# Optimization experiments

Hardware: AMD Instinct MI355X
Metric: run time of the kernel (lower is better)

## Reference

```python
import jax, jax.numpy as jnp
import numpy as np

EPS = 1e-8
NUM_GCN_LAYERS = 2


def _cos(a, b):
    # cosine similarity along last axis, torch.nn.CosineSimilarity semantics
    num = jnp.sum(a * b, axis=-1)
    den = jnp.maximum(jnp.linalg.norm(a, axis=-1) * jnp.linalg.norm(b, axis=-1), EPS)
    return num / den


def _masked_mean(x, mask):
    # x: [..., L, D], mask: [..., L]
    s = jnp.sum(x * mask[..., None], axis=-2)
    d = jnp.maximum(jnp.sum(mask, axis=-1, keepdims=True), 1.0)
    return s / d


def setup_inputs() -> dict:
    key = jax.random.key(0)
    ks = jax.random.split(key, 12)
    B, C, L, D, P, OM, OE, R = 32, 16, 128, 768, 196, 10, 10, 36
    return {
        "mention_text_feature": jax.random.normal(ks[0], (B, L, D), jnp.float32),
        "mention_text_mask": jnp.ones((B, L), jnp.float32),
        "mention_start_pos": jax.random.randint(ks[1], (B,), 0, L),
        "mention_end_pos": jax.random.randint(ks[2], (B,), 0, L),
        "mention_image_feature": jax.random.normal(ks[3], (B, P, D), jnp.float32),
        "mention_object_feature": jax.random.normal(ks[4], (B, OM, R, D), jnp.float32),
        "mention_object_score": jax.random.uniform(ks[5], (B, OM), jnp.float32, 0.1, 1.0),
        "entity_text_feature": jax.random.normal(ks[6], (B, C, L, D), jnp.float32),
        "entity_text_mask": jnp.ones((B, C, L), jnp.float32),
        "entity_image_feature": jax.random.normal(ks[7], (B, C, P, D), jnp.float32),
        "entity_object_feature": jax.random.normal(ks[8], (B, C, OE, R, D), jnp.float32),
        "entity_object_score": jax.random.uniform(ks[9], (B, C, OE), jnp.float32, 0.1, 1.0),
        "miet_similarity": jax.random.normal(ks[10], (B, C), jnp.float32),
        "mtei_similarity": jax.random.normal(ks[11], (B, C), jnp.float32),
    }


def _forward(mtf, mtm, msp, mep, mif, mof, mos, etf, etm, eif, eof, eos, miet, mtei):
    B, L, D = mtf.shape
    C = etf.shape[1]

    # ---- VertexEncoder ----
    v_mt = _masked_mean(mtf, mtm)      # [B, D] mention text vertex
    v_mi = jnp.mean(mif, axis=-2)      # [B, D] mention image vertex
    v_et = _masked_mean(etf, etm)      # [B, C, D] entity text vertex
    v_ei = jnp.mean(eif, axis=-2)      # [B, C, D] entity image vertex

    # ---- EdgeEncoder ----
    # mention final repr: mean of start/end token features (span boundary repr)
    start = jnp.take_along_axis(mtf, msp[:, None, None], axis=1)[:, 0]  # [B, D]
    end = jnp.take_along_axis(mtf, mep[:, None, None], axis=1)[:, 0]    # [B, D]
    m_span = 0.5 * (start + end)
    mtet = _cos(m_span[:, None, :], etf[:, :, 0])  # [B, C] vs entity CLS token

    # miei: the original double python loop over (i, j) object pairs is a
    # weighted average of pairwise cosine sims -> one fused einsum pass.
    m = jnp.mean(mof, axis=-2)         # [B, OM, D]
    e = jnp.mean(eof, axis=-2)         # [B, C, OE, D]
    mn = m / jnp.maximum(jnp.linalg.norm(m, axis=-1, keepdims=True), EPS)
    en = e / jnp.maximum(jnp.linalg.norm(e, axis=-1, keepdims=True), EPS)
    cos_ij = jnp.einsum('bid,bcjd->bcij', mn, en)          # [B, C, OM, OE]
    w = mos[:, None, :, None] * eos[:, :, None, :]          # [B, C, OM, OE]
    miei = jnp.sum(cos_ij * w, axis=(2, 3)) / jnp.sum(w, axis=(2, 3))  # [B, C]

    # ---- GCN layers ----
    edges = [jnp.broadcast_to(x[:, :, None], (B, C, D)) for x in (mtet, mtei, miet, miei)]
    vertexes = [v_mt, v_mi, v_et, v_ei]
    vertex_graph = [[(0, 2), (1, 3)], [(2, 2), (3, 3)], [(0, 0), (2, 1)], [(1, 0), (3, 1)]]
    edge_graph = [(0, 2), (0, 3), (1, 2), (1, 3)]

    def conv_v(edge, v, mention_like):
        msg = edge * (v[:, None, :] if v.ndim == 2 else v)  # [B, C, D]
        return jnp.mean(msg, axis=1) if mention_like else msg

    def conv_e(u, v):
        u2 = u[:, None, :] if u.ndim == 2 else u
        v2 = v[:, None, :] if v.ndim == 2 else v
        return u2 * v2  # [B, C, D]

    for _ in range(NUM_GCN_LAYERS):
        new_v = []
        for k, nbrs in enumerate(vertex_graph):
            mention_like = k < 2  # vertexes 0,1 are [B,D]; 2,3 are [B,C,D]
            acc = conv_v(edges[nbrs[0][0]], vertexes[nbrs[0][1]], mention_like)
            acc = acc + conv_v(edges[nbrs[1][0]], vertexes[nbrs[1][1]], mention_like)
            new_v.append(acc)
        new_e = [conv_e(vertexes[ui], vertexes[vi]) for ui, vi in edge_graph]
        vertexes, edges = new_v, new_e

    mention, entity = vertexes[0], vertexes[2]
    return _cos(mention[:, None, :], entity)  # [B, C]


def reference(mention_text_feature, mention_text_mask, mention_start_pos, mention_end_pos, mention_image_feature, mention_object_feature, mention_object_score, entity_text_feature, entity_text_mask, entity_image_feature, entity_object_feature, entity_object_score, miet_similarity, mtei_similarity):
    return _forward(mention_text_feature, mention_text_mask, mention_start_pos, mention_end_pos, mention_image_feature, mention_object_feature, mention_object_score, entity_text_feature, entity_text_mask, entity_image_feature, entity_object_feature, entity_object_score, miet_similarity, mtei_similarity)
```

## Files before the change

### kernel.cpp

```cpp
#include <hip/hip_runtime.h>

#define EPSF 1e-8f

#define B_  32
#define C_  16
#define L_  128
#define D_  768
#define D4_ 192
#define P_  196
#define OM_ 10
#define OE_ 10
#define R_  36

__device__ __forceinline__ float4 f4add(float4 a, float4 b){
  return make_float4(a.x+b.x, a.y+b.y, a.z+b.z, a.w+b.w);
}
__device__ __forceinline__ float4 f4scale(float4 a, float s){
  return make_float4(a.x*s, a.y*s, a.z*s, a.w*s);
}
__device__ __forceinline__ float f4dot(float4 a, float4 b){
  return a.x*b.x + a.y*b.y + a.z*b.z + a.w*b.w;
}
__device__ __forceinline__ float wave_sum(float v){
  #pragma unroll
  for (int off = 32; off > 0; off >>= 1) v += __shfl_down(v, off);
  return v;
}

__global__ __launch_bounds__(192)
void mof_k(const float* __restrict__ mof, const float* __restrict__ mos,
           float* __restrict__ m_mean, float* __restrict__ q)
{
  int blk = blockIdx.x;
  int t = threadIdx.x, wv = t >> 6, lane = t & 63;
  const float4* inp = (const float4*)mof + (size_t)blk * R_ * D4_;
  float4 acc = make_float4(0.f, 0.f, 0.f, 0.f);
  #pragma unroll 6
  for (int r = 0; r < R_; ++r)
    acc = f4add(acc, inp[(size_t)r * D4_ + t]);
  acc = f4scale(acc, 1.f / 36.f);
  ((float4*)m_mean)[(size_t)blk * D4_ + t] = acc;
  __shared__ float sh[3];
  float n = wave_sum(f4dot(acc, acc));
  if (lane == 0) sh[wv] = n;
  __syncthreads();
  if (t == 0) q[blk] = mos[blk] / fmaxf(sqrtf(sh[0] + sh[1] + sh[2]), EPSF);
}

__global__ __launch_bounds__(192)
void mega2_k(const float* __restrict__ eofp, const float* __restrict__ eif,
             const float* __restrict__ etf, const float* __restrict__ mif,
             const float* __restrict__ mtf,
             const float* __restrict__ etm, const float* __restrict__ mtm,
             const float* __restrict__ m_mean, const float* __restrict__ q,
             const float* __restrict__ eos,
             float* __restrict__ part_eif, float* __restrict__ part_etf,
             float* __restrict__ part_mif, float* __restrict__ part_mtf,
             float* __restrict__ msum, float* __restrict__ p)
{
  int blk = blockIdx.x;
  int t = threadIdx.x;

  if (blk < 1707) {
    int wave = t >> 6, lane = t & 63;
    int g = blk * 3 + wave;
    if (g >= 5120) return;
    int b = g / (C_ * OE_);
    const float4* ep = (const float4*)eofp + (size_t)g * R_ * D4_;
    float4 a0 = make_float4(0,0,0,0), a1 = a0, a2 = a0;
    #pragma unroll 4
    for (int r = 0; r < R_; ++r) {
      const float4* row = ep + (size_t)r * D4_;
      a0 = f4add(a0, row[lane]);
      a1 = f4add(a1, row[lane + 64]);
      a2 = f4add(a2, row[lane + 128]);
    }
    const float inv36 = 1.f / 36.f;
    a0 = f4scale(a0, inv36); a1 = f4scale(a1, inv36); a2 = f4scale(a2, inv36);
    float nrm = f4dot(a0, a0) + f4dot(a1, a1) + f4dot(a2, a2);
    float s = 0.f;
    const float4* mp = (const float4*)m_mean + (size_t)b * OM_ * D4_;
    #pragma unroll
    for (int i = 0; i < OM_; ++i) {
      const float4* mr = mp + (size_t)i * D4_;
      float di = f4dot(a0, mr[lane]) + f4dot(a1, mr[lane + 64]) + f4dot(a2, mr[lane + 128]);
      s += q[b * OM_ + i] * di;
    }
    s = wave_sum(s); nrm = wave_sum(nrm);
    if (lane == 0) p[g] = eos[g] * s / fmaxf(sqrtf(nrm), EPSF);
    return;
  }

  blk -= 1707;
  const float* in; const float* mask = nullptr;
  float* part; float* ms = nullptr;
  int ROWS, CH, RPC;
  if (blk < 3584)      { in = eif; part = part_eif; ROWS = 196; CH = 7; RPC = 28; }
  else if (blk < 5632) { blk -= 3584; in = etf; mask = etm; ms = msum + 128;
                         part = part_etf; ROWS = 128; CH = 4; RPC = 32; }
  else if (blk < 5856) { blk -= 5632; in = mif; part = part_mif; ROWS = 196; CH = 7; RPC = 28; }
  else                 { blk -= 5856; in = mtf; mask = mtm; ms = msum;
                         part = part_mtf; ROWS = 128; CH = 4; RPC = 32; }

  int g = blk / CH, ch = blk - g * CH;
  int r0 = ch * RPC;
  int r1 = r0 + RPC; if (r1 > ROWS) r1 = ROWS;
  const float4* inp = (const float4*)in + (size_t)g * ROWS * D4_;
  float4 acc = make_float4(0.f, 0.f, 0.f, 0.f);
  if (mask) {
    const float* mrow = mask + (size_t)g * ROWS;
    float msacc = 0.f;
    #pragma unroll 4
    for (int r = r0; r < r1; ++r) {
      float w = mrow[r];
      float4 v = inp[(size_t)r * D4_ + t];
      acc.x += v.x * w; acc.y += v.y * w; acc.z += v.z * w; acc.w += v.w * w;
      msacc += w;
    }
    if (t == 0) ms[blk] = msacc;
  } else {
    #pragma unroll 4
    for (int r = r0; r < r1; ++r)
      acc = f4add(acc, inp[(size_t)r * D4_ + t]);
  }
  ((float4*)part)[(size_t)blk * D4_ + t] = acc;
}

__device__ __forceinline__ void combine_body(const float* __restrict__ part,
                                             const float* __restrict__ msum,
                                             float* __restrict__ out,
                                             int secblk, int CH, float invn)
{
  int idx = secblk * 256 + threadIdx.x;
  int g = idx / D4_, t = idx - g * D4_;
  const float4* pp = (const float4*)part + (size_t)(g * CH) * D4_ + t;
  float4 acc = make_float4(0.f, 0.f, 0.f, 0.f);
  for (int ch = 0; ch < CH; ++ch) acc = f4add(acc, pp[(size_t)ch * D4_]);
  float scale;
  if (msum) {
    float s = 0.f;
    for (int ch = 0; ch < CH; ++ch) s += msum[g * CH + ch];
    scale = 1.f / fmaxf(s, 1.f);
  } else scale = invn;
  ((float4*)out)[idx] = f4scale(acc, scale);
}

__global__ __launch_bounds__(256)
void comb2_k(const float* __restrict__ part_eif, const float* __restrict__ part_etf,
             const float* __restrict__ part_mif, const float* __restrict__ part_mtf,
             const float* __restrict__ msum,
             const float* __restrict__ etf, const float* __restrict__ mtf,
             const int* __restrict__ msp, const int* __restrict__ mep,
             float* __restrict__ v_ei, float* __restrict__ v_et,
             float* __restrict__ v_mi, float* __restrict__ v_mt,
             float* __restrict__ mtet)
{
  int blk = blockIdx.x;
  if (blk < 384)       { combine_body(part_eif, nullptr, v_ei, blk, 7, 1.f/196.f); return; }
  else if (blk < 768)  { combine_body(part_etf, msum + 128, v_et, blk - 384, 4, 0.f); return; }
  else if (blk < 792)  { combine_body(part_mif, nullptr, v_mi, blk - 768, 7, 1.f/196.f); return; }
  else if (blk < 816)  { combine_body(part_mtf, msum, v_mt, blk - 792, 4, 0.f); return; }
  else {
    int w = (blk - 816) * 4 + (threadIdx.x >> 6);
    int lane = threadIdx.x & 63;
    int b = w >> 4;
    const float4* ecls = (const float4*)etf + (size_t)w * L_ * D4_;
    const float4* mb   = (const float4*)mtf + (size_t)b * L_ * D4_;
    int sp = msp[b], ep = mep[b];
    float dt = 0.f, na = 0.f, nb = 0.f;
    #pragma unroll
    for (int k = 0; k < 3; ++k) {
      float4 a = f4scale(f4add(mb[(size_t)sp * D4_ + lane + 64*k],
                               mb[(size_t)ep * D4_ + lane + 64*k]), 0.5f);
      float4 e = ecls[lane + 64*k];
      dt += f4dot(a, e); na += f4dot(a, a); nb += f4dot(e, e);
    }
    dt = wave_sum(dt); na = wave_sum(na); nb = wave_sum(nb);
    if (lane == 0) mtet[w] = dt / fmaxf(sqrtf(na) * sqrtf(nb), EPSF);
  }
}

__global__ __launch_bounds__(256)
void tail_k(const float* __restrict__ p, const float* __restrict__ mos,
            const float* __restrict__ eos,
            const float* __restrict__ v_mt, const float* __restrict__ v_mi,
            const float* __restrict__ v_et, const float* __restrict__ v_ei,
            const float* __restrict__ mtet, const float* __restrict__ mtei,
            const float* __restrict__ miet,
            float* __restrict__ out)
{
  __shared__ float sh_e0[C_], sh_e1[C_], sh_e2[C_], sh_e3[C_];
  __shared__ float4 sh_m4[D4_], sh_s4[D4_];
  int b = blockIdx.x, tid = threadIdx.x;

  if (tid < C_) {
    int bc = b * C_ + tid;
    float num = 0.f, se = 0.f, sm = 0.f;
    #pragma unroll
    for (int j = 0; j < OE_; ++j) { num += p[bc * OE_ + j]; se += eos[bc * OE_ + j]; }
    #pragma unroll
    for (int i = 0; i < OM_; ++i) sm += mos[b * OM_ + i];
    sh_e3[tid] = num / (sm * se);
    sh_e0[tid] = mtet[bc];
    sh_e1[tid] = mtei[bc];
    sh_e2[tid] = miet[bc];
  }
  __syncthreads();

  const float invC = 1.f / (float)C_;
  for (int d = tid; d < D_; d += 256) {
    float vmt = v_mt[b * D_ + d], vmi = v_mi[b * D_ + d];
    float nv0 = 0.f, nv1 = 0.f, macc = 0.f;
    #pragma unroll
    for (int c = 0; c < C_; ++c) {
      int bc = b * C_ + c;
      float et = v_et[(size_t)bc * D_ + d];
      float ei = v_ei[(size_t)bc * D_ + d];
      float e0 = sh_e0[c], e1 = sh_e1[c], e2 = sh_e2[c], e3 = sh_e3[c];
      nv0 += e0 * et + e1 * ei;
      nv1 += e2 * et + e3 * ei;
      macc += (vmt * et) * (e0 * vmt + e2 * vmi)
            + (vmt * ei) * (e1 * vmt + e3 * vmi);
    }
    ((float*)sh_m4)[d] = macc * invC;
    ((float*)sh_s4)[d] = vmt * (nv0 * invC) + vmi * (nv1 * invC);
  }
  __syncthreads();

  int wv = tid >> 6, lane = tid & 63;
  for (int c = wv; c < C_; c += 4) {
    const float4* ep = (const float4*)v_et + (size_t)(b * C_ + c) * D4_;
    float dt = 0.f, nm = 0.f, ne = 0.f;
    #pragma unroll
    for (int k = 0; k < 3; ++k) {
      float4 m = sh_m4[lane + 64*k];
      float4 sv = sh_s4[lane + 64*k];
      float4 e = ep[lane + 64*k];
      float4 ent = make_float4(e.x * sv.x, e.y * sv.y, e.z * sv.z, e.w * sv.w);
      dt += f4dot(m, ent); nm += f4dot(m, m); ne += f4dot(ent, ent);
    }
    dt = wave_sum(dt); nm = wave_sum(nm); ne = wave_sum(ne);
    if (lane == 0) out[b * C_ + c] = dt / fmaxf(sqrtf(nm) * sqrtf(ne), EPSF);
  }
}

extern "C" void kernel_launch(void* const* d_in, const int* in_sizes, int n_in,
                              void* d_out, int out_size, void* d_ws, size_t ws_size,
                              hipStream_t stream)
{
  const float* mtf  = (const float*)d_in[0];
  const float* mtm  = (const float*)d_in[1];
  const int*   msp  = (const int*)  d_in[2];
  const int*   mep  = (const int*)  d_in[3];
  const float* mif  = (const float*)d_in[4];
  const float* mof  = (const float*)d_in[5];
  const float* mos  = (const float*)d_in[6];
  const float* etf  = (const float*)d_in[7];
  const float* etm  = (const float*)d_in[8];
  const float* eif  = (const float*)d_in[9];
  const float* eofp = (const float*)d_in[10];
  const float* eos  = (const float*)d_in[11];
  const float* miet = (const float*)d_in[12];
  const float* mtei = (const float*)d_in[13];
  float* out = (float*)d_out;
  float* ws = (float*)d_ws;

  float* PART_EIF = ws;
  float* PART_ETF = PART_EIF + 2752512;
  float* PART_MIF = PART_ETF + 1572864;
  float* PART_MTF = PART_MIF + 172032;
  float* MSUM     = PART_MTF + 98304;
  float* M_MEAN   = MSUM     + 2176;
  float* Q        = M_MEAN   + 245760;
  float* V_MT     = Q        + 512;
  float* V_MI     = V_MT     + 24576;
  float* V_ET     = V_MI     + 24576;
  float* V_EI     = V_ET     + 393216;
  float* MTET     = V_EI     + 393216;
  float* P_BUF    = MTET     + 512;

  mof_k<<<320, 192, 0, stream>>>(mof, mos, M_MEAN, Q);

  mega2_k<<<7691, 192, 0, stream>>>(eofp, eif, etf, mif, mtf, etm, mtm,
                                    M_MEAN, Q, eos,
                                    PART_EIF, PART_ETF, PART_MIF, PART_MTF,
                                    MSUM, P_BUF);

  comb2_k<<<944, 256, 0, stream>>>(PART_EIF, PART_ETF, PART_MIF, PART_MTF,
                                   MSUM, etf, mtf, msp, mep,
                                   V_EI, V_ET, V_MI, V_MT, MTET);

  tail_k<<<B_, 256, 0, stream>>>(P_BUF, mos, eos, V_MT, V_MI, V_ET, V_EI,
                                 MTET, mtei, miet, out);
}
```

Measured before the change: 226.0 us.

## Restructure into three kernels with two-chunk partials and fused final combine

Moves the mention image/text means and the CLS cosine into the first kernel alongside the object means. The entity image and text reductions now use two chunks per group instead of 7 and 4. The separate combine kernel is removed: the last kernel sums the two partials directly, keeping entity text vertices in shared memory. All streaming reads use nontemporal loads. The aim is fewer launches and less partial-buffer traffic, at the cost of fewer blocks for the large reductions and a heavier final kernel running only 32 blocks.

```diff
diff --git a/kernel.cpp b/kernel.cpp
--- a/kernel.cpp
+++ b/kernel.cpp
@@ -12,77 +12,139 @@
 #define OE_ 10
 #define R_  36
 
-__device__ __forceinline__ float4 f4add(float4 a, float4 b){
-  return make_float4(a.x+b.x, a.y+b.y, a.z+b.z, a.w+b.w);
-}
-__device__ __forceinline__ float4 f4scale(float4 a, float s){
-  return make_float4(a.x*s, a.y*s, a.z*s, a.w*s);
-}
-__device__ __forceinline__ float f4dot(float4 a, float4 b){
-  return a.x*b.x + a.y*b.y + a.z*b.z + a.w*b.w;
-}
+typedef float f4 __attribute__((ext_vector_type(4)));
+
+__device__ __forceinline__ float f4dot(f4 a, f4 b){ return a.x*b.x + a.y*b.y + a.z*b.z + a.w*b.w; }
+__device__ __forceinline__ f4 ldnt(const f4* p){ return __builtin_nontemporal_load(p); }
 __device__ __forceinline__ float wave_sum(float v){
   #pragma unroll
   for (int off = 32; off > 0; off >>= 1) v += __shfl_down(v, off);
   return v;
 }
 
+__global__ __launch_bounds__(384)
+void d1_k(const float* __restrict__ mof, const float* __restrict__ mos,
+          const float* __restrict__ mif, const float* __restrict__ mtf,
+          const float* __restrict__ mtm, const float* __restrict__ etf,
+          const int* __restrict__ msp, const int* __restrict__ mep,
+          float* __restrict__ m_mean, float* __restrict__ q,
+          float* __restrict__ v_mi, float* __restrict__ v_mt,
+          float* __restrict__ mtet)
+{
+  __shared__ f4 shv[2][D4_];
+  __shared__ float shs[4];
+  int blk = blockIdx.x, t = threadIdx.x;
+
+  if (blk < 320) {
+    int g = blk;
+    int half = t / D4_, col = t - half * D4_;
+    const f4* base = (const f4*)mof + (size_t)g * R_ * D4_;
+    f4 acc = {0.f, 0.f, 0.f, 0.f};
+    int r0 = half * 18;
+    #pragma unroll 6
+    for (int r = r0; r < r0 + 18; ++r) acc += ldnt(base + (size_t)r * D4_ + col);
+    shv[half][col] = acc;
+    __syncthreads();
+    if (t < D4_) {
+      f4 mean = (shv[0][col] + shv[1][col]) * (1.f / 36.f);
+      ((f4*)m_mean)[(size_t)g * D4_ + col] = mean;
+      float n = wave_sum(f4dot(mean, mean));
+      if ((t & 63) == 0) shs[t >> 6] = n;
+    }
+    __syncthreads();
+    if (t == 0) q[g] = mos[g] / fmaxf(sqrtf(shs[0] + shs[1] + shs[2]), EPSF);
+    return;
+  }
+  if (blk < 352) {
+    int b = blk - 320;
+    int half = t / D4_, col = t - half * D4_;
+    const f4* base = (const f4*)mif + (size_t)b * P_ * D4_;
+    f4 acc = {0.f, 0.f, 0.f, 0.f};
+    int r0 = half * 98;
+    #pragma unroll 4
+    for (int r = r0; r < r0 + 98; ++r) acc += ldnt(base + (size_t)r * D4_ + col);
+    shv[half][col] = acc;
+    __syncthreads();
+    if (t < D4_)
+      ((f4*)v_mi)[(size_t)b * D4_ + col] = (shv[0][col] + shv[1][col]) * (1.f / 196.f);
+    return;
+  }
+  if (blk < 384) {
+    int b = blk - 352;
+    int half = t / D4_, col = t - half * D4_;
+    const f4* base = (const f4*)mtf + (size_t)b * L_ * D4_;
+    const float* mrow = mtm + (size_t)b * L_;
+    f4 acc = {0.f, 0.f, 0.f, 0.f};
+    float ms = 0.f;
+    int r0 = half * 64;
+    #pragma unroll 4
+    for (int r = r0; r < r0 + 64; ++r) {
+      float w = mrow[r];
+      acc += ldnt(base + (size_t)r * D4_ + col) * w;
+      ms += w;
+    }
+    shv[half][col] = acc;
+    if (t == 0)    shs[0] = ms;
+    if (t == D4_)  shs[1] = ms;
+    __syncthreads();
+    if (t < D4_) {
+      float scale = 1.f / fmaxf(shs[0] + shs[1], 1.f);
+      ((f4*)v_mt)[(size_t)b * D4_ + col] = (shv[0][col] + shv[1][col]) * scale;
+    }
+    return;
+  }
+  {
+    int w = (blk - 384) * 6 + (t >> 6);
+    if (w >= B_ * C_) return;
+    int lane = t & 63;
+    int b = w >> 4;
+    const f4* ecls = (const f4*)etf + (size_t)w * L_ * D4_;
+    const f4* mb   = (const f4*)mtf + (size_t)b * L_ * D4_;
+    int sp = msp[b], ep = mep[b];
+    float dt = 0.f, na = 0.f, nb = 0.f;
+    #pragma unroll
+    for (int k = 0; k < 3; ++k) {
+      f4 a = (mb[(size_t)sp * D4_ + lane + 64*k] + mb[(size_t)ep * D4_ + lane + 64*k]) * 0.5f;
+      f4 e = ecls[lane + 64*k];
+      dt += f4dot(a, e); na += f4dot(a, a); nb += f4dot(e, e);
+    }
+    dt = wave_sum(dt); na = wave_sum(na); nb = wave_sum(nb);
+    if (lane == 0) mtet[w] = dt / fmaxf(sqrtf(na) * sqrtf(nb), EPSF);
+  }
+}
+
 __global__ __launch_bounds__(192)
-void mof_k(const float* __restrict__ mof, const float* __restrict__ mos,
-           float* __restrict__ m_mean, float* __restrict__ q)
-{
-  int blk = blockIdx.x;
-  int t = threadIdx.x, wv = t >> 6, lane = t & 63;
-  const float4* inp = (const float4*)mof + (size_t)blk * R_ * D4_;
-  float4 acc = make_float4(0.f, 0.f, 0.f, 0.f);
-  #pragma unroll 6
-  for (int r = 0; r < R_; ++r)
-    acc = f4add(acc, inp[(size_t)r * D4_ + t]);
-  acc = f4scale(acc, 1.f / 36.f);
-  ((float4*)m_mean)[(size_t)blk * D4_ + t] = acc;
-  __shared__ float sh[3];
-  float n = wave_sum(f4dot(acc, acc));
-  if (lane == 0) sh[wv] = n;
-  __syncthreads();
-  if (t == 0) q[blk] = mos[blk] / fmaxf(sqrtf(sh[0] + sh[1] + sh[2]), EPSF);
-}
-
-__global__ __launch_bounds__(192)
-void mega2_k(const float* __restrict__ eofp, const float* __restrict__ eif,
-             const float* __restrict__ etf, const float* __restrict__ mif,
-             const float* __restrict__ mtf,
-             const float* __restrict__ etm, const float* __restrict__ mtm,
-             const float* __restrict__ m_mean, const float* __restrict__ q,
-             const float* __restrict__ eos,
-             float* __restrict__ part_eif, float* __restrict__ part_etf,
-             float* __restrict__ part_mif, float* __restrict__ part_mtf,
-             float* __restrict__ msum, float* __restrict__ p)
-{
-  int blk = blockIdx.x;
-  int t = threadIdx.x;
+void d2_k(const float* __restrict__ eofp, const float* __restrict__ eif,
+          const float* __restrict__ etf, const float* __restrict__ etm,
+          const float* __restrict__ m_mean, const float* __restrict__ q,
+          const float* __restrict__ eos,
+          float* __restrict__ part_eif, float* __restrict__ part_etf,
+          float* __restrict__ msum_etf, float* __restrict__ p)
+{
+  int blk = blockIdx.x, t = threadIdx.x;
 
   if (blk < 1707) {
     int wave = t >> 6, lane = t & 63;
     int g = blk * 3 + wave;
-    if (g >= 5120) return;
+    if (g >= B_ * C_ * OE_) return;
     int b = g / (C_ * OE_);
-    const float4* ep = (const float4*)eofp + (size_t)g * R_ * D4_;
-    float4 a0 = make_float4(0,0,0,0), a1 = a0, a2 = a0;
+    const f4* ep = (const f4*)eofp + (size_t)g * R_ * D4_;
+    f4 a0 = {0.f,0.f,0.f,0.f}, a1 = a0, a2 = a0;
     #pragma unroll 4
     for (int r = 0; r < R_; ++r) {
-      const float4* row = ep + (size_t)r * D4_;
-      a0 = f4add(a0, row[lane]);
-      a1 = f4add(a1, row[lane + 64]);
-      a2 = f4add(a2, row[lane + 128]);
+      const f4* row = ep + (size_t)r * D4_;
+      a0 += ldnt(row + lane);
+      a1 += ldnt(row + lane + 64);
+      a2 += ldnt(row + lane + 128);
     }
     const float inv36 = 1.f / 36.f;
-    a0 = f4scale(a0, inv36); a1 = f4scale(a1, inv36); a2 = f4scale(a2, inv36);
+    a0 *= inv36; a1 *= inv36; a2 *= inv36;
     float nrm = f4dot(a0, a0) + f4dot(a1, a1) + f4dot(a2, a2);
     float s = 0.f;
-    const float4* mp = (const float4*)m_mean + (size_t)b * OM_ * D4_;
+    const f4* mp = (const f4*)m_mean + (size_t)b * OM_ * D4_;
     #pragma unroll
     for (int i = 0; i < OM_; ++i) {
-      const float4* mr = mp + (size_t)i * D4_;
+      const f4* mr = mp + (size_t)i * D4_;
       float di = f4dot(a0, mr[lane]) + f4dot(a1, mr[lane + 64]) + f4dot(a2, mr[lane + 128]);
       s += q[b * OM_ + i] * di;
     }
@@ -90,153 +152,103 @@
     if (lane == 0) p[g] = eos[g] * s / fmaxf(sqrtf(nrm), EPSF);
     return;
   }
-
   blk -= 1707;
-  const float* in; const float* mask = nullptr;
-  float* part; float* ms = nullptr;
-  int ROWS, CH, RPC;
-  if (blk < 3584)      { in = eif; part = part_eif; ROWS = 196; CH = 7; RPC = 28; }
-  else if (blk < 5632) { blk -= 3584; in = etf; mask = etm; ms = msum + 128;
-                         part = part_etf; ROWS = 128; CH = 4; RPC = 32; }
-  else if (blk < 5856) { blk -= 5632; in = mif; part = part_mif; ROWS = 196; CH = 7; RPC = 28; }
-  else                 { blk -= 5856; in = mtf; mask = mtm; ms = msum;
-                         part = part_mtf; ROWS = 128; CH = 4; RPC = 32; }
-
-  int g = blk / CH, ch = blk - g * CH;
-  int r0 = ch * RPC;
-  int r1 = r0 + RPC; if (r1 > ROWS) r1 = ROWS;
-  const float4* inp = (const float4*)in + (size_t)g * ROWS * D4_;
-  float4 acc = make_float4(0.f, 0.f, 0.f, 0.f);
-  if (mask) {
-    const float* mrow = mask + (size_t)g * ROWS;
-    float msacc = 0.f;
-    #pragma unroll 4
-    for (int r = r0; r < r1; ++r) {
+  if (blk < 1024) {
+    int g = blk >> 1, ch = blk & 1;
+    const f4* inp = (const f4*)eif + ((size_t)g * P_ + ch * 98) * D4_;
+    f4 acc = {0.f,0.f,0.f,0.f};
+    #pragma unroll 4
+    for (int r = 0; r < 98; ++r) acc += ldnt(inp + (size_t)r * D4_ + t);
+    ((f4*)part_eif)[(size_t)blk * D4_ + t] = acc;
+    return;
+  }
+  blk -= 1024;
+  {
+    int g = blk >> 1, ch = blk & 1;
+    const f4* inp = (const f4*)etf + ((size_t)g * L_ + ch * 64) * D4_;
+    const float* mrow = etm + (size_t)g * L_ + ch * 64;
+    f4 acc = {0.f,0.f,0.f,0.f};
+    float ms = 0.f;
+    #pragma unroll 4
+    for (int r = 0; r < 64; ++r) {
       float w = mrow[r];
-      float4 v = inp[(size_t)r * D4_ + t];
-      acc.x += v.x * w; acc.y += v.y * w; acc.z += v.z * w; acc.w += v.w * w;
-      msacc += w;
-    }
-    if (t == 0) ms[blk] = msacc;
-  } else {
-    #pragma unroll 4
-    for (int r = r0; r < r1; ++r)
-      acc = f4add(acc, inp[(size_t)r * D4_ + t]);
-  }
-  ((float4*)part)[(size_t)blk * D4_ + t] = acc;
-}
-
-__device__ __forceinline__ void combine_body(const float* __restrict__ part,
-                                             const float* __restrict__ msum,
-                                             float* __restrict__ out,
-                                             int secblk, int CH, float invn)
-{
-  int idx = secblk * 256 + threadIdx.x;
-  int g = idx / D4_, t = idx - g * D4_;
-  const float4* pp = (const float4*)part + (size_t)(g * CH) * D4_ + t;
-  float4 acc = make_float4(0.f, 0.f, 0.f, 0.f);
-  for (int ch = 0; ch < CH; ++ch) acc = f4add(acc, pp[(size_t)ch * D4_]);
-  float scale;
-  if (msum) {
-    float s = 0.f;
-    for (int ch = 0; ch < CH; ++ch) s += msum[g * CH + ch];
-    scale = 1.f / fmaxf(s, 1.f);
-  } else scale = invn;
-  ((float4*)out)[idx] = f4scale(acc, scale);
-}
-
-__global__ __launch_bounds__(256)
-void comb2_k(const float* __restrict__ part_eif, const float* __restrict__ part_etf,
-             const float* __restrict__ part_mif, const float* __restrict__ part_mtf,
-             const float* __restrict__ msum,
-             const float* __restrict__ etf, const float* __restrict__ mtf,
-             const int* __restrict__ msp, const int* __restrict__ mep,
-             float* __restrict__ v_ei, float* __restrict__ v_et,
-             float* __restrict__ v_mi, float* __restrict__ v_mt,
-             float* __restrict__ mtet)
-{
-  int blk = blockIdx.x;
-  if (blk < 384)       { combine_body(part_eif, nullptr, v_ei, blk, 7, 1.f/196.f); return; }
-  else if (blk < 768)  { combine_body(part_etf, msum + 128, v_et, blk - 384, 4, 0.f); return; }
-  else if (blk < 792)  { combine_body(part_mif, nullptr, v_mi, blk - 768, 7, 1.f/196.f); return; }
-  else if (blk < 816)  { combine_body(part_mtf, msum, v_mt, blk - 792, 4, 0.f); return; }
-  else {
-    int w = (blk - 816) * 4 + (threadIdx.x >> 6);
-    int lane = threadIdx.x & 63;
-    int b = w >> 4;
-    const float4* ecls = (const float4*)etf + (size_t)w * L_ * D4_;
-    const float4* mb   = (const float4*)mtf + (size_t)b * L_ * D4_;
-    int sp = msp[b], ep = mep[b];
-    float dt = 0.f, na = 0.f, nb = 0.f;
-    #pragma unroll
-    for (int k = 0; k < 3; ++k) {
-      float4 a = f4scale(f4add(mb[(size_t)sp * D4_ + lane + 64*k],
-                               mb[(size_t)ep * D4_ + lane + 64*k]), 0.5f);
-      float4 e = ecls[lane + 64*k];
-      dt += f4dot(a, e); na += f4dot(a, a); nb += f4dot(e, e);
-    }
-    dt = wave_sum(dt); na = wave_sum(na); nb = wave_sum(nb);
-    if (lane == 0) mtet[w] = dt / fmaxf(sqrtf(na) * sqrtf(nb), EPSF);
-  }
-}
-
-__global__ __launch_bounds__(256)
-void tail_k(const float* __restrict__ p, const float* __restrict__ mos,
-            const float* __restrict__ eos,
-            const float* __restrict__ v_mt, const float* __restrict__ v_mi,
-            const float* __restrict__ v_et, const float* __restrict__ v_ei,
-            const float* __restrict__ mtet, const float* __restrict__ mtei,
-            const float* __restrict__ miet,
-            float* __restrict__ out)
-{
+      acc += ldnt(inp + (size_t)r * D4_ + t) * w;
+      ms += w;
+    }
+    ((f4*)part_etf)[(size_t)blk * D4_ + t] = acc;
+    if (t == 0) msum_etf[blk] = ms;
+  }
+}
+
+__global__ __launch_bounds__(384)
+void d3_k(const float* __restrict__ part_eif, const float* __restrict__ part_etf,
+          const float* __restrict__ msum_etf,
+          const float* __restrict__ p, const float* __restrict__ mos,
+          const float* __restrict__ eos,
+          const float* __restrict__ v_mt, const float* __restrict__ v_mi,
+          const float* __restrict__ mtet, const float* __restrict__ mtei,
+          const float* __restrict__ miet,
+          float* __restrict__ out)
+{
+  __shared__ float s_vet[C_][D_];
   __shared__ float sh_e0[C_], sh_e1[C_], sh_e2[C_], sh_e3[C_];
-  __shared__ float4 sh_m4[D4_], sh_s4[D4_];
-  int b = blockIdx.x, tid = threadIdx.x;
-
-  if (tid < C_) {
-    int bc = b * C_ + tid;
+  __shared__ float sh_m[D_], sh_s[D_];
+  int b = blockIdx.x, t = threadIdx.x;
+
+  for (int it = t; it < C_ * D4_; it += 384) {
+    int c = it / D4_, col = it - c * D4_;
+    int i2 = (b * C_ + c) * 2;
+    f4 a = ((const f4*)part_etf)[(size_t)i2 * D4_ + col]
+         + ((const f4*)part_etf)[(size_t)(i2 + 1) * D4_ + col];
+    float scale = 1.f / fmaxf(msum_etf[i2] + msum_etf[i2 + 1], 1.f);
+    ((f4*)&s_vet[c][0])[col] = a * scale;
+  }
+  if (t < C_) {
+    int bc = b * C_ + t;
     float num = 0.f, se = 0.f, sm = 0.f;
     #pragma unroll
     for (int j = 0; j < OE_; ++j) { num += p[bc * OE_ + j]; se += eos[bc * OE_ + j]; }
     #pragma unroll
     for (int i = 0; i < OM_; ++i) sm += mos[b * OM_ + i];
-    sh_e3[tid] = num / (sm * se);
-    sh_e0[tid] = mtet[bc];
-    sh_e1[tid] = mtei[bc];
-    sh_e2[tid] = miet[bc];
+    sh_e3[t] = num / (sm * se);
+    sh_e0[t] = mtet[bc];
+    sh_e1[t] = mtei[bc];
+    sh_e2[t] = miet[bc];
   }
   __syncthreads();
 
-  const float invC = 1.f / (float)C_;
-  for (int d = tid; d < D_; d += 256) {
+  const float invC = 1.f / (float)C_, inv196 = 1.f / 196.f;
+  for (int d = t; d < D_; d += 384) {
     float vmt = v_mt[b * D_ + d], vmi = v_mi[b * D_ + d];
     float nv0 = 0.f, nv1 = 0.f, macc = 0.f;
     #pragma unroll
     for (int c = 0; c < C_; ++c) {
-      int bc = b * C_ + c;
-      float et = v_et[(size_t)bc * D_ + d];
-      float ei = v_ei[(size_t)bc * D_ + d];
+      int i2 = (b * C_ + c) * 2;
+      float et = s_vet[c][d];
+      float ei = (part_eif[(size_t)i2 * D_ + d] + part_eif[(size_t)(i2 + 1) * D_ + d]) * inv196;
       float e0 = sh_e0[c], e1 = sh_e1[c], e2 = sh_e2[c], e3 = sh_e3[c];
       nv0 += e0 * et + e1 * ei;
       nv1 += e2 * et + e3 * ei;
       macc += (vmt * et) * (e0 * vmt + e2 * vmi)
             + (vmt * ei) * (e1 * vmt + e3 * vmi);
     }
-    ((float*)sh_m4)[d] = macc * invC;
-    ((float*)sh_s4)[d] = vmt * (nv0 * invC) + vmi * (nv1 * invC);
+    sh_m[d] = macc * invC;
+    sh_s[d] = vmt * (nv0 * invC) + vmi * (nv1 * invC);
   }
   __syncthreads();
 
-  int wv = tid >> 6, lane = tid & 63;
-  for (int c = wv; c < C_; c += 4) {
-    const float4* ep = (const float4*)v_et + (size_t)(b * C_ + c) * D4_;
+  int wv = t >> 6, lane = t & 63;
+  for (int c = wv; c < C_; c += 6) {
+    const f4* ep = (const f4*)&s_vet[c][0];
+    const f4* mp = (const f4*)sh_m;
+    const f4* sp = (const f4*)sh_s;
     float dt = 0.f, nm = 0.f, ne = 0.f;
     #pragma unroll
     for (int k = 0; k < 3; ++k) {
-      float4 m = sh_m4[lane + 64*k];
-      float4 sv = sh_s4[lane + 64*k];
-      float4 e = ep[lane + 64*k];
-      float4 ent = make_float4(e.x * sv.x, e.y * sv.y, e.z * sv.z, e.w * sv.w);
+      f4 m = mp[lane + 64*k];
+      f4 sv = sp[lane + 64*k];
+      f4 e = ep[lane + 64*k];
+      f4 ent = e * sv;
       dt += f4dot(m, ent); nm += f4dot(m, m); ne += f4dot(ent, ent);
     }
     dt = wave_sum(dt); nm = wave_sum(nm); ne = wave_sum(ne);
@@ -266,30 +278,21 @@
   float* ws = (float*)d_ws;
 
   float* PART_EIF = ws;
-  float* PART_ETF = PART_EIF + 2752512;
-  float* PART_MIF = PART_ETF + 1572864;
-  float* PART_MTF = PART_MIF + 172032;
-  float* MSUM     = PART_MTF + 98304;
-  float* M_MEAN   = MSUM     + 2176;
+  float* PART_ETF = PART_EIF + 786432;
+  float* MSUM_ETF = PART_ETF + 786432;
+  float* M_MEAN   = MSUM_ETF + 2048;
   float* Q        = M_MEAN   + 245760;
-  float* V_MT     = Q        + 512;
+  float* V_MT     = Q        + 320;
   float* V_MI     = V_MT     + 24576;
-  float* V_ET     = V_MI     + 24576;
-  float* V_EI     = V_ET     + 393216;
-  float* MTET     = V_EI     + 393216;
+  float* MTET     = V_MI     + 24576;
   float* P_BUF    = MTET     + 512;
 
-  mof_k<<<320, 192, 0, stream>>>(mof, mos, M_MEAN, Q);
-
-  mega2_k<<<7691, 192, 0, stream>>>(eofp, eif, etf, mif, mtf, etm, mtm,
-                                    M_MEAN, Q, eos,
-                                    PART_EIF, PART_ETF, PART_MIF, PART_MTF,
-                                    MSUM, P_BUF);
-
-  comb2_k<<<944, 256, 0, stream>>>(PART_EIF, PART_ETF, PART_MIF, PART_MTF,
-                                   MSUM, etf, mtf, msp, mep,
-                                   V_EI, V_ET, V_MI, V_MT, MTET);
-
-  tail_k<<<B_, 256, 0, stream>>>(P_BUF, mos, eos, V_MT, V_MI, V_ET, V_EI,
-                                 MTET, mtei, miet, out);
-}
+  d1_k<<<470, 384, 0, stream>>>(mof, mos, mif, mtf, mtm, etf, msp, mep,
+                                M_MEAN, Q, V_MI, V_MT, MTET);
+
+  d2_k<<<3755, 192, 0, stream>>>(eofp, eif, etf, etm, M_MEAN, Q, eos,
+                                 PART_EIF, PART_ETF, MSUM_ETF, P_BUF);
+
+  d3_k<<<B_, 384, 0, stream>>>(PART_EIF, PART_ETF, MSUM_ETF, P_BUF, mos, eos,
+                               V_MT, V_MI, MTET, mtei, miet, out);
+}
```

After: 210.8 us. 1.07x faster.
